# Performance work log

Measured on AMD Instinct MI355X. Metric: run time of the kernel, lower is better.

Reference implementation:

```python
import jax, jax.numpy as jnp
import numpy as np

B, S, W, D, A = 64, 512, 256, 768, 32


def setup_inputs() -> dict:
    key = jax.random.key(0)
    k1, k2, k3 = jax.random.split(key, 3)
    sequence_output = jax.random.normal(k1, (B, S, D), dtype=jnp.float32)
    # head-subword indices per example (valid, sorted, in [0, S))
    word_idxs = jnp.sort(jax.random.randint(k2, (B, W), 0, S), axis=-1)
    cls_w = jax.random.normal(k3, (A, 3, D), dtype=jnp.float32) * 0.02
    cls_b = jnp.zeros((A, 3), dtype=jnp.float32)
    return {"sequence_output": sequence_output, "word_idxs": word_idxs,
            "cls_w": cls_w, "cls_b": cls_b}


def reference(sequence_output, word_idxs, cls_w, cls_b):
    # Original builds a [B, W, S] one-hot pooler matrix and does bmm with
    # sequence_output [B, S, D]; since rows are one-hot at word head positions,
    # this is exactly a gather along the subword axis.
    pooled = jnp.take_along_axis(sequence_output, word_idxs[..., None], axis=1)  # [B, W, D]
    # dropout is identity at inference. Fused per-attribute Linear(768, 3):
    logits = jnp.einsum("bwd,acd->abwc", pooled, cls_w) + cls_b[:, None, None, :]  # [A, B, W, 3]
    return logits
```

## Files before the change

### kernel.cpp

```cpp
#include <hip/hip_runtime.h>
#include <hip/hip_bf16.h>

#define B_    64
#define S_    512
#define W_    256
#define D_    768
#define NATTR 32
#define NN    96

typedef __attribute__((ext_vector_type(8))) short bfrag;
typedef __attribute__((ext_vector_type(4))) float f32x4;

static __device__ __forceinline__ short f2bf(float f) {
  __hip_bfloat16 h = __float2bfloat16(f);
  return __builtin_bit_cast(short, h);
}

static __device__ __forceinline__ bfrag cvt8(f32x4 lo, f32x4 hi) {
  bfrag r;
  r[0] = f2bf(lo[0]); r[1] = f2bf(lo[1]); r[2] = f2bf(lo[2]); r[3] = f2bf(lo[3]);
  r[4] = f2bf(hi[0]); r[5] = f2bf(hi[1]); r[6] = f2bf(hi[2]); r[7] = f2bf(hi[3]);
  return r;
}

__global__ __launch_bounds__(256, 2) void ner_mfma_kernel(
    const float* __restrict__ seq, const int* __restrict__ widx,
    const float* __restrict__ cw, const float* __restrict__ cb,
    float* __restrict__ out)
{
  __shared__ float lds[32][NN + 1];

  const int tid  = threadIdx.x;
  const int lane = tid & 63;
  const int wv   = tid >> 6;
  const int r16  = lane & 15;
  const int g    = lane >> 4;

  const int blk = blockIdx.x;
  const int b   = blk >> 3;
  const int w0  = (blk & 7) << 5;

  const int msub = wv & 1;
  const int nh   = wv >> 1;

  const int wl   = w0 + msub * 16 + r16;
  const int sidx = widx[b * W_ + wl];
  const float* arow = seq + ((size_t)b * S_ + sidx) * D_ + g * 8;

  const int nb = nh * 48 + r16;
  const float* b0p = cw + (size_t)(nb +  0) * D_ + g * 8;
  const float* b1p = cw + (size_t)(nb + 16) * D_ + g * 8;
  const float* b2p = cw + (size_t)(nb + 32) * D_ + g * 8;

  f32x4 acc0 = {0.f,0.f,0.f,0.f};
  f32x4 acc1 = {0.f,0.f,0.f,0.f};
  f32x4 acc2 = {0.f,0.f,0.f,0.f};

  for (int kk = 0; kk < D_; kk += 32) {
    f32x4 alo  = *(const f32x4*)(arow + kk);
    f32x4 ahi  = *(const f32x4*)(arow + kk + 4);
    f32x4 b0lo = *(const f32x4*)(b0p + kk);
    f32x4 b0hi = *(const f32x4*)(b0p + kk + 4);
    f32x4 b1lo = *(const f32x4*)(b1p + kk);
    f32x4 b1hi = *(const f32x4*)(b1p + kk + 4);
    f32x4 b2lo = *(const f32x4*)(b2p + kk);
    f32x4 b2hi = *(const f32x4*)(b2p + kk + 4);
    bfrag af = cvt8(alo, ahi);
    acc0 = __builtin_amdgcn_mfma_f32_16x16x32_bf16(af, cvt8(b0lo, b0hi), acc0, 0, 0, 0);
    acc1 = __builtin_amdgcn_mfma_f32_16x16x32_bf16(af, cvt8(b1lo, b1hi), acc1, 0, 0, 0);
    acc2 = __builtin_amdgcn_mfma_f32_16x16x32_bf16(af, cvt8(b2lo, b2hi), acc2, 0, 0, 0);
  }

  {
    const int wl0 = msub * 16 + g * 4;
    const float bias0 = cb[nh * 48 +      r16];
    const float bias1 = cb[nh * 48 + 16 + r16];
    const float bias2 = cb[nh * 48 + 32 + r16];
    #pragma unroll
    for (int j = 0; j < 4; ++j) {
      lds[wl0 + j][nh * 48 +      r16] = acc0[j] + bias0;
      lds[wl0 + j][nh * 48 + 16 + r16] = acc1[j] + bias1;
      lds[wl0 + j][nh * 48 + 32 + r16] = acc2[j] + bias2;
    }
  }
  __syncthreads();

  #pragma unroll
  for (int it = 0; it < 3; ++it) {
    const int f4i = tid + it * 256;
    const int a   = f4i / 24;
    const int e0  = (f4i % 24) * 4;
    float vv[4];
    #pragma unroll
    for (int u = 0; u < 4; ++u) {
      const int e = e0 + u;
      vv[u] = lds[e / 3][a * 3 + e % 3];
    }
    float* op = out + ((size_t)(a * B_ + b) * W_ + w0) * 3 + e0;
    *(float4*)op = make_float4(vv[0], vv[1], vv[2], vv[3]);
  }
}

extern "C" void kernel_launch(void* const* d_in, const int* in_sizes, int n_in,
                              void* d_out, int out_size, void* d_ws, size_t ws_size,
                              hipStream_t stream) {
  const float* seq  = (const float*)d_in[0];
  const int*   widx = (const int*)d_in[1];
  const float* cw   = (const float*)d_in[2];
  const float* cb   = (const float*)d_in[3];
  float* out = (float*)d_out;

  dim3 grid(B_ * (W_ / 32));
  dim3 block(256);
  ner_mfma_kernel<<<grid, block, 0, stream>>>(seq, widx, cw, cb, out);
}
```

Measured before the change: 168.0 us.

## Stage gathered rows and weights through swizzled LDS with 768-thread blocks

Replaces per-lane strided global loads feeding MFMA directly with cooperative, coalesced loads of 64-wide K chunks of the gathered activation rows and all 96 weight rows. The chunks are converted to bf16 once and stored in XOR-swizzled shared memory, with register prefetch of the next chunk. Blocks grow to 12 waves, each computing a single 16x16 output tile, so weights are loaded once per block instead of redundantly per wave. The cost is two barriers per K chunk and higher LDS use, and a launch-bounds hint that may constrain register allocation.

Measured after the change: 143.5 us. -14.6%, faster.

```diff
diff --git a/kernel.cpp b/kernel.cpp
--- a/kernel.cpp
+++ b/kernel.cpp
@@ -5,96 +5,112 @@
 #define S_    512
 #define W_    256
 #define D_    768
-#define NATTR 32
 #define NN    96
+#define BK    64
+#define NCH   12
 
 typedef __attribute__((ext_vector_type(8))) short bfrag;
 typedef __attribute__((ext_vector_type(4))) float f32x4;
+typedef __attribute__((ext_vector_type(4))) short s16x4;
 
 static __device__ __forceinline__ short f2bf(float f) {
   __hip_bfloat16 h = __float2bfloat16(f);
   return __builtin_bit_cast(short, h);
 }
-
-static __device__ __forceinline__ bfrag cvt8(f32x4 lo, f32x4 hi) {
-  bfrag r;
-  r[0] = f2bf(lo[0]); r[1] = f2bf(lo[1]); r[2] = f2bf(lo[2]); r[3] = f2bf(lo[3]);
-  r[4] = f2bf(hi[0]); r[5] = f2bf(hi[1]); r[6] = f2bf(hi[2]); r[7] = f2bf(hi[3]);
+static __device__ __forceinline__ s16x4 pack4(f32x4 v) {
+  s16x4 r;
+  r[0] = f2bf(v[0]); r[1] = f2bf(v[1]); r[2] = f2bf(v[2]); r[3] = f2bf(v[3]);
   return r;
 }
 
-__global__ __launch_bounds__(256, 2) void ner_mfma_kernel(
+__global__ __launch_bounds__(768, 6) void ner_kernel(
     const float* __restrict__ seq, const int* __restrict__ widx,
     const float* __restrict__ cw, const float* __restrict__ cb,
     float* __restrict__ out)
 {
-  __shared__ float lds[32][NN + 1];
+  __shared__ union {
+    struct {
+      short a[32 * 64];
+      short b[96 * 64];
+    } s;
+    float o[32 * 100];
+  } u;
 
-  const int tid  = threadIdx.x;
-  const int lane = tid & 63;
-  const int wv   = tid >> 6;
-  const int r16  = lane & 15;
-  const int g    = lane >> 4;
-
+  const int tid = threadIdx.x;
   const int blk = blockIdx.x;
   const int b   = blk >> 3;
   const int w0  = (blk & 7) << 5;
 
-  const int msub = wv & 1;
-  const int nh   = wv >> 1;
+  const int srow = tid >> 4;
+  const int kc   = tid & 15;
+  const float* aptr = nullptr;
+  if (tid < 512) {
+    const int sidx = widx[b * W_ + w0 + srow];
+    aptr = seq + ((size_t)b * S_ + sidx) * D_ + kc * 4;
+  }
+  const int brow1 = srow + 48;
+  const float* bptr0 = cw + (size_t)srow  * D_ + kc * 4;
+  const float* bptr1 = cw + (size_t)brow1 * D_ + kc * 4;
 
-  const int wl   = w0 + msub * 16 + r16;
-  const int sidx = widx[b * W_ + wl];
-  const float* arow = seq + ((size_t)b * S_ + sidx) * D_ + g * 8;
+  const int lane = tid & 63;
+  const int wv   = tid >> 6;
+  const int mt   = wv & 1;
+  const int nt   = wv >> 1;
+  const int r16  = lane & 15;
+  const int g    = lane >> 4;
 
-  const int nb = nh * 48 + r16;
-  const float* b0p = cw + (size_t)(nb +  0) * D_ + g * 8;
-  const float* b1p = cw + (size_t)(nb + 16) * D_ + g * 8;
-  const float* b2p = cw + (size_t)(nb + 32) * D_ + g * 8;
+  const int am = mt * 16 + r16;
+  const int bn = nt * 16 + r16;
 
-  f32x4 acc0 = {0.f,0.f,0.f,0.f};
-  f32x4 acc1 = {0.f,0.f,0.f,0.f};
-  f32x4 acc2 = {0.f,0.f,0.f,0.f};
+  f32x4 acc = {0.f, 0.f, 0.f, 0.f};
 
-  for (int kk = 0; kk < D_; kk += 32) {
-    f32x4 alo  = *(const f32x4*)(arow + kk);
-    f32x4 ahi  = *(const f32x4*)(arow + kk + 4);
-    f32x4 b0lo = *(const f32x4*)(b0p + kk);
-    f32x4 b0hi = *(const f32x4*)(b0p + kk + 4);
-    f32x4 b1lo = *(const f32x4*)(b1p + kk);
-    f32x4 b1hi = *(const f32x4*)(b1p + kk + 4);
-    f32x4 b2lo = *(const f32x4*)(b2p + kk);
-    f32x4 b2hi = *(const f32x4*)(b2p + kk + 4);
-    bfrag af = cvt8(alo, ahi);
-    acc0 = __builtin_amdgcn_mfma_f32_16x16x32_bf16(af, cvt8(b0lo, b0hi), acc0, 0, 0, 0);
-    acc1 = __builtin_amdgcn_mfma_f32_16x16x32_bf16(af, cvt8(b1lo, b1hi), acc1, 0, 0, 0);
-    acc2 = __builtin_amdgcn_mfma_f32_16x16x32_bf16(af, cvt8(b2lo, b2hi), acc2, 0, 0, 0);
+  char* const la = (char*)u.s.a;
+  char* const lb = (char*)u.s.b;
+
+  f32x4 ra, rb0, rb1;
+  if (tid < 512) ra = *(const f32x4*)(aptr);
+  rb0 = *(const f32x4*)(bptr0);
+  rb1 = *(const f32x4*)(bptr1);
+
+  for (int c = 0; c < NCH; ++c) {
+    __syncthreads();
+    if (tid < 512)
+      *(s16x4*)(la + srow  * 128 + ((kc * 8) ^ ((srow  & 7) << 4))) = pack4(ra);
+    *(s16x4*)(lb + srow  * 128 + ((kc * 8) ^ ((srow  & 7) << 4))) = pack4(rb0);
+    *(s16x4*)(lb + brow1 * 128 + ((kc * 8) ^ ((brow1 & 7) << 4))) = pack4(rb1);
+    __syncthreads();
+    if (c + 1 < NCH) {
+      const int k0 = (c + 1) * BK;
+      if (tid < 512) ra = *(const f32x4*)(aptr + k0);
+      rb0 = *(const f32x4*)(bptr0 + k0);
+      rb1 = *(const f32x4*)(bptr1 + k0);
+    }
+    #pragma unroll
+    for (int ks = 0; ks < 2; ++ks) {
+      bfrag af = *(const bfrag*)(la + am * 128 + (((ks * 64) + g * 16) ^ ((am & 7) << 4)));
+      bfrag bf = *(const bfrag*)(lb + bn * 128 + (((ks * 64) + g * 16) ^ ((bn & 7) << 4)));
+      acc = __builtin_amdgcn_mfma_f32_16x16x32_bf16(af, bf, acc, 0, 0, 0);
+    }
   }
 
+  __syncthreads();
   {
-    const int wl0 = msub * 16 + g * 4;
-    const float bias0 = cb[nh * 48 +      r16];
-    const float bias1 = cb[nh * 48 + 16 + r16];
-    const float bias2 = cb[nh * 48 + 32 + r16];
+    const int n    = nt * 16 + r16;
+    const float bias = cb[n];
+    const int row0 = mt * 16 + g * 4;
     #pragma unroll
-    for (int j = 0; j < 4; ++j) {
-      lds[wl0 + j][nh * 48 +      r16] = acc0[j] + bias0;
-      lds[wl0 + j][nh * 48 + 16 + r16] = acc1[j] + bias1;
-      lds[wl0 + j][nh * 48 + 32 + r16] = acc2[j] + bias2;
-    }
+    for (int j = 0; j < 4; ++j)
+      u.o[(row0 + j) * 100 + n] = acc[j] + bias;
   }
   __syncthreads();
-
-  #pragma unroll
-  for (int it = 0; it < 3; ++it) {
-    const int f4i = tid + it * 256;
-    const int a   = f4i / 24;
-    const int e0  = (f4i % 24) * 4;
+  {
+    const int a  = tid / 24;
+    const int e0 = (tid % 24) * 4;
     float vv[4];
     #pragma unroll
-    for (int u = 0; u < 4; ++u) {
-      const int e = e0 + u;
-      vv[u] = lds[e / 3][a * 3 + e % 3];
+    for (int q = 0; q < 4; ++q) {
+      const int e = e0 + q;
+      vv[q] = u.o[(e / 3) * 100 + a * 3 + (e - (e / 3) * 3)];
     }
     float* op = out + ((size_t)(a * B_ + b) * W_ + w0) * 3 + e0;
     *(float4*)op = make_float4(vv[0], vv[1], vv[2], vv[3]);
@@ -111,6 +127,6 @@
   float* out = (float*)d_out;
 
   dim3 grid(B_ * (W_ / 32));
-  dim3 block(256);
-  ner_mfma_kernel<<<grid, block, 0, stream>>>(seq, widx, cw, cb, out);
+  dim3 block(768);
+  ner_kernel<<<grid, block, 0, stream>>>(seq, widx, cw, cb, out);
 }
```
